# Performance work log

Hardware: AMD Instinct MI355X
Metric: run time of the kernel (lower is better)

## Reference

```python
import jax, jax.numpy as jnp
import numpy as np

B, N, IN, E, H, F = 64, 256, 128, 256, 8, 1024


def setup_inputs() -> dict:
    key = jax.random.key(0)
    ks = jax.random.split(key, 16)
    x = jax.random.normal(ks[0], (B, N, IN), jnp.float32)
    adj = (jax.random.uniform(ks[1], (B, N, N)) < 0.1).astype(jnp.float32)
    adj = jnp.maximum(adj, adj.transpose(0, 2, 1))  # symmetric 0/1 adjacency
    mask = jax.random.randint(ks[2], (B, N), 0, 2).astype(jnp.float32)
    dist = jax.random.normal(ks[3], (B, N, N), jnp.float32)

    def lin(k, i, o):
        return (jax.random.normal(k, (i, o), jnp.float32) / np.sqrt(i)).astype(jnp.float32)

    return dict(
        x=x, adj=adj, mask=mask, dist=dist,
        W1=lin(ks[4], IN, E), b1=jnp.zeros((E,), jnp.float32),
        W2=lin(ks[5], E, E), b2=jnp.zeros((E,), jnp.float32),
        W3=lin(ks[6], E, E), b3=jnp.zeros((E,), jnp.float32),
        ln1_g=jnp.ones((E,), jnp.float32), ln1_b=jnp.zeros((E,), jnp.float32),
        Wq=lin(ks[7], E, H * E), Wk=lin(ks[8], E, H * E), Wv=lin(ks[9], E, H * E),
        Wo=lin(ks[10], H * E, E), bo=jnp.zeros((E,), jnp.float32),
        ln2_g=jnp.ones((E,), jnp.float32), ln2_b=jnp.zeros((E,), jnp.float32),
        Wf1=lin(ks[11], E, F), bf1=jnp.zeros((F,), jnp.float32),
        Wf2=lin(ks[12], F, E), bf2=jnp.zeros((E,), jnp.float32),
    )


def _layernorm(x, g, b):
    m = x.mean(-1, keepdims=True)
    v = ((x - m) ** 2).mean(-1, keepdims=True)
    return (x - m) * jax.lax.rsqrt(v + 1e-5) * g + b


def reference(x, adj, mask, dist, W1, b1, W2, b2, W3, b3, ln1_g, ln1_b,
              Wq, Wk, Wv, Wo, bo, ln2_g, ln2_b, Wf1, bf1, Wf2, bf2):
    # --- DenseGCNConv normalization (add self-loops, sym-normalize) ---
    eye = jnp.eye(N, dtype=adj.dtype)
    A = adj * (1.0 - eye) + eye                      # fill_diag(adj, 1)
    dis = jax.lax.rsqrt(jnp.clip(A.sum(-1), 1.0, None))
    An = dis[:, :, None] * A * dis[:, None, :]       # D^-1/2 A D^-1/2, [B,N,N]
    m3 = mask[:, :, None]

    def gcn(h, W, b):
        return (jnp.einsum('bij,bjf->bif', An, h @ W) + b) * m3

    g1 = jax.nn.relu(gcn(x, W1, b1))
    g2 = jax.nn.relu(gcn(g1, W2, b2))
    g3 = jax.nn.relu(gcn(g2, W3, b3))
    gcn_res = g1 + g2 + g3

    # --- masked MHA with distance bias (head dim = E per head) ---
    h = _layernorm(gcn_res, ln1_g, ln1_b)
    mh = mask[:, None, :, None]                      # [B,1,N,1]
    q = (h @ Wq).reshape(B, N, H, E).transpose(0, 2, 1, 3) * mh
    k = (h @ Wk).reshape(B, N, H, E).transpose(0, 2, 1, 3) * mh
    v = (h @ Wv).reshape(B, N, H, E).transpose(0, 2, 1, 3) * mh
    a = jnp.einsum('bhne,bhme->bhnm', q * (E ** -0.5), k) + dist[:, None]
    am = (mask[:, :, None] * mask[:, None, :])[:, None]  # [B,1,N,N]
    a = jnp.where(am == 0, -1e9, a)
    a = jax.nn.softmax(a, axis=-1)
    a = jnp.where(am == 0, 0.0, a)
    y = jnp.einsum('bhnm,bhme->bhne', a, v).transpose(0, 2, 1, 3).reshape(B, N, H * E)
    y = (y @ Wo + bo) * m3
    att = gcn_res + y

    # --- FFN block ---
    f = _layernorm(att, ln2_g, ln2_b)
    f = (jax.nn.gelu(f @ Wf1 + bf1, approximate=False) @ Wf2 + bf2) * m3
    att = att + f
    return gcn_res + att
```

## Files before the change

kernel.cpp:

```cpp
#include <hip/hip_runtime.h>
#include <hip/hip_bf16.h>
#include <cmath>

#define BB 64
#define NNODES 256
#define INF_ 128
#define EE 256
#define HH 8
#define FFN 1024
#define BNROWS 16384

typedef __attribute__((ext_vector_type(8))) short short8;
typedef __attribute__((ext_vector_type(4))) float floatx4;
typedef __attribute__((ext_vector_type(4))) unsigned short ushort4v;

__device__ __forceinline__ float b2f(unsigned short u) {
  union { unsigned u32; float f; } w; w.u32 = ((unsigned)u) << 16; return w.f;
}
__device__ __forceinline__ unsigned short f2b(float f) {
  union { float f; unsigned u32; } w; w.f = f;
  unsigned r = w.u32 + 0x7FFFu + ((w.u32 >> 16) & 1u);
  return (unsigned short)(r >> 16);
}
__device__ __forceinline__ float gelu_f(float x) {
  const float z = 0.7978845608028654f * (x + 0.044715f * x * x * x);
  const float e = __expf(2.0f * z);
  const float th = (e - 1.0f) / (e + 1.0f);
  return 0.5f * x * (1.0f + th);
}

typedef const __attribute__((address_space(1))) void GV;
typedef __attribute__((address_space(3))) void LV;

__device__ __forceinline__ void gl_lds16(const unsigned short* g,
                                         unsigned short* l, int lane) {
#if __has_builtin(__builtin_amdgcn_global_load_lds)
  __builtin_amdgcn_global_load_lds((GV*)g, (LV*)l, 16, 0, 0);
#else
  *(short8*)(l + lane * 8) = *(const short8*)g;
#endif
}

struct PackArgs {
  const float* src[12];
  unsigned short* dst[12];
  int R[12], C[12];
  int start[13];
};

__launch_bounds__(256)
__global__ void pack_kernel(PackArgs a)
{
  __shared__ float tile[32][33];
  const int bid = blockIdx.x;
  int j = 0;
  while (bid >= a.start[j + 1]) j++;
  const int lb = bid - a.start[j];
  const float* src = a.src[j];
  unsigned short* dst = a.dst[j];
  const int R = a.R[j], C = a.C[j];

  if (C == 0) {
    const int i = (lb * 256 + threadIdx.x) * 4;
    if (i >= R) return;
    floatx4 v = *(const floatx4*)(src + i);
    ushort4v o;
    #pragma unroll
    for (int k = 0; k < 4; k++) o[k] = f2b(v[k]);
    *(ushort4v*)(dst + i) = o;
    return;
  }
  const int tpr = C >> 5;
  const int c0 = (lb % tpr) * 32, r0 = (lb / tpr) * 32;
  const int tx = threadIdx.x & 31, ty = threadIdx.x >> 5;
  #pragma unroll
  for (int i = ty; i < 32; i += 8)
    tile[i][tx] = src[(long long)(r0 + i) * C + c0 + tx];
  __syncthreads();
  #pragma unroll
  for (int i = ty; i < 32; i += 8)
    dst[(long long)(c0 + i) * R + r0 + tx] = f2b(tile[tx][i]);
}

__launch_bounds__(1024)
__global__ void an_kernel(const float* __restrict__ adj,
                          unsigned short* __restrict__ An)
{
  __shared__ float dis[256];
  const int b = blockIdx.x;
  const float* A = adj + (long long)b * 65536;
  const int t = threadIdx.x;
  const int row = t >> 2, seg = t & 3;
  const float* p = A + row * 256 + seg * 64;
  float s = 0.f;
  for (int k = 0; k < 64; k += 4) {
    floatx4 v = *(const floatx4*)(p + k);
    #pragma unroll
    for (int jj = 0; jj < 4; jj++) {
      const int col = seg * 64 + k + jj;
      s += (col == row) ? 1.0f : v[jj];
    }
  }
  s += __shfl_xor(s, 1);
  s += __shfl_xor(s, 2);
  if (seg == 0) dis[row] = 1.0f / sqrtf(fmaxf(s, 1.0f));
  __syncthreads();
  const float di = dis[row];
  unsigned short* dst = An + (long long)b * 65536 + row * 256 + seg * 64;
  for (int k = 0; k < 64; k += 4) {
    floatx4 v = *(const floatx4*)(p + k);
    ushort4v o;
    #pragma unroll
    for (int jj = 0; jj < 4; jj++) {
      const int col = seg * 64 + k + jj;
      o[jj] = f2b(di * dis[col] * ((col == row) ? 1.0f : v[jj]));
    }
    *(ushort4v*)(dst + k) = o;
  }
}

__launch_bounds__(512, 4)
__global__ void gemm_kernel(const unsigned short* __restrict__ A, int lda,
                            long long sAo, long long sAi,
                            const unsigned short* __restrict__ Bm, int ldb,
                            long long sBo, long long sBi,
                            void* __restrict__ Cv, int ldc,
                            long long sCo, long long sCi,
                            int K, int zshift, int mode, int flag,
                            const float* __restrict__ aux1,
                            const float* __restrict__ mask,
                            float* __restrict__ gcn,
                            void* __restrict__ aux2)
{
  __shared__ __align__(16) unsigned short sA[16384];
  __shared__ __align__(16) unsigned short sB[16384];

  const int t = threadIdx.x;
  const int z = blockIdx.z;
  const int zi = z & ((1 << zshift) - 1);
  const int zb = z >> zshift;
  const int m0 = blockIdx.x * 128;
  const int n0 = blockIdx.y * 128;
  A  += zb * sAo + zi * sAi;
  Bm += zb * sBo + zi * sBi;
  const long long cbase = zb * sCo + zi * sCi;

  const int lane = t & 63;
  const int w = t >> 6;
  const int wm = w >> 2, wn = w & 3;
  const int lm = lane & 15, qd = lane >> 4;

  floatx4 acc[4][2] = {};

  const int sub = lane >> 4;
  const int qs  = lane & 15;
  const unsigned short* pA[4];
  const unsigned short* pB[4];
  #pragma unroll
  for (int i = 0; i < 4; i++) {
    const int d = w * 4 + i;
    const int r = d * 4 + sub;
    const int co = (qs ^ (r & 7)) * 8;
    pA[i] = A + (long long)(m0 + r) * lda + co;
    pB[i] = Bm + (long long)(n0 + r) * ldb + co;
  }

  for (int kk = 0; kk < K; kk += 128) {
    #pragma unroll
    for (int i = 0; i < 4; i++) {
      gl_lds16(pA[i] + kk, &sA[(w * 4 + i) * 512], lane);
      gl_lds16(pB[i] + kk, &sB[(w * 4 + i) * 512], lane);
    }
    __syncthreads();

    #pragma unroll
    for (int ks = 0; ks < 4; ks++) {
      short8 af[4], bg[2];
      const int q = ks * 4 + qd;
      #pragma unroll
      for (int mi = 0; mi < 4; mi++) {
        const int r = wm * 64 + mi * 16 + lm;
        af[mi] = *(const short8*)&sA[r * 128 + ((q ^ (r & 7)) * 8)];
      }
      #pragma unroll
      for (int ni = 0; ni < 2; ni++) {
        const int r = wn * 32 + ni * 16 + lm;
        bg[ni] = *(const short8*)&sB[r * 128 + ((q ^ (r & 7)) * 8)];
      }
      #pragma unroll
      for (int mi = 0; mi < 4; mi++)
        #pragma unroll
        for (int ni = 0; ni < 2; ni++)
          acc[mi][ni] = __builtin_amdgcn_mfma_f32_16x16x32_bf16(
              af[mi], bg[ni], acc[mi][ni], 0, 0, 0);
    }
    __syncthreads();
  }

  #pragma unroll
  for (int mi = 0; mi < 4; mi++) {
    const int row0 = m0 + wm * 64 + mi * 16 + qd * 4;
    #pragma unroll
    for (int ni = 0; ni < 2; ni++) {
      const int col = n0 + wn * 32 + ni * 16 + lm;
      floatx4 a = acc[mi][ni];
      if (mode == 0) {
        float* Cf = (float*)Cv;
        #pragma unroll
        for (int r = 0; r < 4; r++)
          Cf[cbase + (long long)(row0 + r) * ldc + col] = a[r];
      } else if (mode == 1) {
        unsigned short* Cb = (unsigned short*)Cv;
        #pragma unroll
        for (int r = 0; r < 4; r++)
          Cb[cbase + (long long)(row0 + r) * ldc + col] = f2b(a[r]);
      } else if (mode == 2) {
        float* Cf = (float*)Cv;
        #pragma unroll
        for (int r = 0; r < 4; r++)
          Cf[cbase + (long long)(row0 + r) * ldc + col] += a[r];
      } else if (mode == 3) {
        unsigned short* Cb = (unsigned short*)Cv;
        const float bv = aux1[col];
        #pragma unroll
        for (int r = 0; r < 4; r++)
          Cb[cbase + (long long)(row0 + r) * ldc + col] = f2b(gelu_f(a[r] + bv));
      } else if (mode == 5) {
        const int b = row0 >> 8, n = row0 & 255;
        ushort4v o;
        #pragma unroll
        for (int r = 0; r < 4; r++) o[r] = f2b(a[r]);
        *(ushort4v*)((unsigned short*)Cv + (long long)b * 65536 + col * 256 + n) = o;
      } else if (mode == 8) {
        float* Cf = (float*)Cv;
        const float* attf = (const float*)aux2;
        const float bv = aux1[col];
        #pragma unroll
        for (int r = 0; r < 4; r++) {
          const long long idx = (long long)(row0 + r) * 256 + col;
          Cf[idx] = gcn[idx] + attf[idx] + (a[r] + bv) * mask[row0 + r];
        }
      } else if (mode == 9) {
        const int token = zb * 256 + col;
        const float m = mask[token];
        ushort4v o; floatx4 g;
        #pragma unroll
        for (int r = 0; r < 4; r++) {
          const float v = fmaxf((a[r] + aux1[row0 + r]) * m, 0.f);
          o[r] = f2b(v); g[r] = v;
        }
        *(ushort4v*)((unsigned short*)Cv + (long long)token * 256 + row0) = o;
        float* gp = gcn + (long long)token * 256 + row0;
        if (flag) { floatx4 old = *(const floatx4*)gp; g += old; }
        *(floatx4*)gp = g;
      } else if (mode == 12) {
        float* Cf = (float*)Cv;
        const float bv = aux1[col];
        #pragma unroll
        for (int r = 0; r < 4; r++) {
          const long long idx = (long long)(row0 + r) * 256 + col;
          Cf[idx] = gcn[idx] + (a[r] + bv) * mask[row0 + r];
        }
      } else if (mode == 13) {
        unsigned short* Cb = (unsigned short*)Cv;
        #pragma unroll
        for (int r = 0; r < 4; r++)
          Cb[cbase + (long long)(row0 + r) * ldc + col] = f2b(a[r] * 0.0625f);
      } else {
        if (col < 2048) {
          unsigned short* Cb = (unsigned short*)Cv;
          #pragma unroll
          for (int r = 0; r < 4; r++)
            Cb[(long long)(row0 + r) * 2048 + col] = f2b(a[r]);
        } else {
          const int z2 = (row0 >> 8) * 8 + ((col >> 8) - 8);
          const int e = col & 255, n = row0 & 255;
          ushort4v o;
          #pragma unroll
          for (int r = 0; r < 4; r++) o[r] = f2b(a[r]);
          *(ushort4v*)((unsigned short*)aux2 + (long long)z2 * 65536 + e * 256 + n) = o;
        }
      }
    }
  }
}

__launch_bounds__(512, 2)
__global__ void attn_kernel(unsigned short* __restrict__ QP,
                            const unsigned short* __restrict__ HBF,
                            const unsigned short* __restrict__ VT,
                            const unsigned short* __restrict__ DSTB,
                            const float* __restrict__ mask)
{
  __shared__ __align__(16) unsigned short sA8[8192];
  __shared__ __align__(16) unsigned short sB16[16384];
  __shared__ float redm[4][128];
  __shared__ float reds[4][128];

  const int mt = blockIdx.x;
  const int z  = blockIdx.y;
  const int b  = z >> 3, h = z & 7;
  const int t = threadIdx.x, lane = t & 63, w = t >> 6;
  const int wm = w >> 2, wn = w & 3;
  const int lm = lane & 15, qd = lane >> 4;
  const int m0 = mt * 128;

  unsigned short* Qm = QP + ((long long)(b * 256 + m0)) * 2048 + h * 256;
  const unsigned short* Hb = HBF + ((long long)b) * 65536;
  const unsigned short* Vb = VT + (long long)z * 65536;
  const unsigned short* db = DSTB + (long long)b * 65536;
  const float* maskb = mask + b * 256;

  const int rin = lane >> 3;
  const int qs  = lane & 7;

  floatx4 S[4][4] = {};
  for (int c = 0; c < 4; c++) {
    const int e0 = c * 64;
    #pragma unroll
    for (int i = 0; i < 2; i++) {
      const int d = w * 2 + i;
      const int r = d * 8 + rin;
      gl_lds16(Qm + (long long)r * 2048 + e0 + ((qs ^ (r & 7)) * 8),
               &sA8[d * 512], lane);
    }
    #pragma unroll
    for (int i = 0; i < 4; i++) {
      const int d = w * 4 + i;
      const int r = d * 8 + rin;
      gl_lds16(Hb + (long long)r * 256 + e0 + ((qs ^ (r & 7)) * 8),
               &sB16[d * 512], lane);
    }
    __syncthreads();
    #pragma unroll
    for (int ks = 0; ks < 2; ks++) {
      short8 af[4], bg4[4];
      const int o = ks * 4 + qd;
      #pragma unroll
      for (int mi = 0; mi < 4; mi++) {
        const int r = wm * 64 + mi * 16 + lm;
        af[mi] = *(const short8*)&sA8[r * 64 + ((o ^ (r & 7)) * 8)];
      }
      #pragma unroll
      for (int ni = 0; ni < 4; ni++) {
        const int r = wn * 64 + ni * 16 + lm;
        bg4[ni] = *(const short8*)&sB16[r * 64 + ((o ^ (r & 7)) * 8)];
      }
      #pragma unroll
      for (int mi = 0; mi < 4; mi++)
        #pragma unroll
        for (int ni = 0; ni < 4; ni++)
          S[mi][ni] = __builtin_amdgcn_mfma_f32_16x16x32_bf16(
              af[mi], bg4[ni], S[mi][ni], 0, 0, 0);
    }
    __syncthreads();
  }

  #pragma unroll
  for (int i = 0; i < 4; i++) {
    const int d = w * 4 + i;
    const int r = d * 8 + rin;
    gl_lds16(Vb + (long long)r * 256 + ((qs ^ (r & 7)) * 8),
             &sB16[d * 512], lane);
  }

  float mk[4];
  #pragma unroll
  for (int ni = 0; ni < 4; ni++) mk[ni] = maskb[wn * 64 + ni * 16 + lm];

  float lred[4][4];
  #pragma unroll
  for (int mi = 0; mi < 4; mi++) {
    #pragma unroll
    for (int r = 0; r < 4; r++) {
      const int row = wm * 64 + mi * 16 + qd * 4 + r;
      const float mq = maskb[m0 + row];
      float mx = -3e38f;
      #pragma unroll
      for (int ni = 0; ni < 4; ni++) {
        const int col = wn * 64 + ni * 16 + lm;
        const float dv = b2f(db[(long long)(m0 + row) * 256 + col]);
        const float v = (mq != 0.f && mk[ni] != 0.f) ? (S[mi][ni][r] + dv) : -1e9f;
        S[mi][ni][r] = v;
        mx = fmaxf(mx, v);
      }
      lred[mi][r] = mx;
    }
  }
  #pragma unroll
  for (int off = 1; off < 16; off <<= 1)
    #pragma unroll
    for (int mi = 0; mi < 4; mi++)
      #pragma unroll
      for (int r = 0; r < 4; r++)
        lred[mi][r] = fmaxf(lred[mi][r], __shfl_xor(lred[mi][r], off));
  if (lm == 0)
    #pragma unroll
    for (int mi = 0; mi < 4; mi++)
      #pragma unroll
      for (int r = 0; r < 4; r++)
        redm[wn][wm * 64 + mi * 16 + qd * 4 + r] = lred[mi][r];
  __syncthreads();

  #pragma unroll
  for (int mi = 0; mi < 4; mi++) {
    #pragma unroll
    for (int r = 0; r < 4; r++) {
      const int row = wm * 64 + mi * 16 + qd * 4 + r;
      const float gmax = fmaxf(fmaxf(redm[0][row], redm[1][row]),
                               fmaxf(redm[2][row], redm[3][row]));
      float s = 0.f;
      #pragma unroll
      for (int ni = 0; ni < 4; ni++) {
        const float e = __expf(S[mi][ni][r] - gmax);
        S[mi][ni][r] = e;
        s += e;
      }
      lred[mi][r] = s;
    }
  }
  #pragma unroll
  for (int off = 1; off < 16; off <<= 1)
    #pragma unroll
    for (int mi = 0; mi < 4; mi++)
      #pragma unroll
      for (int r = 0; r < 4; r++)
        lred[mi][r] += __shfl_xor(lred[mi][r], off);
  if (lm == 0)
    #pragma unroll
    for (int mi = 0; mi < 4; mi++)
      #pragma unroll
      for (int r = 0; r < 4; r++)
        reds[wn][wm * 64 + mi * 16 + qd * 4 + r] = lred[mi][r];
  __syncthreads();

  #pragma unroll
  for (int mi = 0; mi < 4; mi++) {
    #pragma unroll
    for (int r = 0; r < 4; r++) {
      const int row = wm * 64 + mi * 16 + qd * 4 + r;
      const float gs = reds[0][row] + reds[1][row] + reds[2][row] + reds[3][row];
      const float inv = 1.0f / gs;
      #pragma unroll
      for (int ni = 0; ni < 4; ni++) S[mi][ni][r] *= inv;
    }
  }

  floatx4 Y[4][4] = {};
  for (int c = 0; c < 4; c++) {
    if (wn == c) {
      #pragma unroll
      for (int mi = 0; mi < 4; mi++)
        #pragma unroll
        for (int r = 0; r < 4; r++) {
          const int row = wm * 64 + mi * 16 + qd * 4 + r;
          #pragma unroll
          for (int ni = 0; ni < 4; ni++) {
            const int kl = ni * 16 + lm;
            const int slot = (kl >> 3) ^ (row & 7);
            sA8[row * 64 + slot * 8 + (kl & 7)] = f2b(S[mi][ni][r]);
          }
        }
    }
    __syncthreads();
    #pragma unroll
    for (int ks = 0; ks < 2; ks++) {
      short8 af[4], bg4[4];
      const int o = ks * 4 + qd;
      #pragma unroll
      for (int mi = 0; mi < 4; mi++) {
        const int r = wm * 64 + mi * 16 + lm;
        af[mi] = *(const short8*)&sA8[r * 64 + ((o ^ (r & 7)) * 8)];
      }
      #pragma unroll
      for (int ni = 0; ni < 4; ni++) {
        const int r = wn * 64 + ni * 16 + lm;
        bg4[ni] = *(const short8*)&sB16[r * 64 + ((o ^ (r & 7)) * 8)];
      }
      #pragma unroll
      for (int mi = 0; mi < 4; mi++)
        #pragma unroll
        for (int ni = 0; ni < 4; ni++)
          Y[mi][ni] = __builtin_amdgcn_mfma_f32_16x16x32_bf16(
              af[mi], bg4[ni], Y[mi][ni], 0, 0, 0);
    }
    __syncthreads();
    if (c < 3) {
      #pragma unroll
      for (int i = 0; i < 4; i++) {
        const int d = w * 4 + i;
        const int r = d * 8 + rin;
        gl_lds16(Vb + (long long)r * 256 + (c + 1) * 64 + ((qs ^ (r & 7)) * 8),
                 &sB16[d * 512], lane);
      }
    }
  }

  #pragma unroll
  for (int mi = 0; mi < 4; mi++)
    #pragma unroll
    for (int ni = 0; ni < 4; ni++) {
      const int col = wn * 64 + ni * 16 + lm;
      #pragma unroll
      for (int r = 0; r < 4; r++) {
        const int row = wm * 64 + mi * 16 + qd * 4 + r;
        Qm[(long long)row * 2048 + col] = f2b(Y[mi][ni][r]);
      }
    }
}

__global__ void ln_kernel(const float* __restrict__ X,
                          const float* __restrict__ gam,
                          const float* __restrict__ bet,
                          unsigned short* __restrict__ out)
{
  const int g = blockIdx.x * 4 + (threadIdx.x >> 6);
  const int lane = threadIdx.x & 63;
  floatx4 v = *(const floatx4*)(X + (long long)g * 256 + lane * 4);
  float s = v[0] + v[1] + v[2] + v[3];
  float sq = v[0]*v[0] + v[1]*v[1] + v[2]*v[2] + v[3]*v[3];
  #pragma unroll
  for (int off = 32; off > 0; off >>= 1) {
    s  += __shfl_xor(s, off);
    sq += __shfl_xor(sq, off);
  }
  const float mean = s * (1.0f / 256.0f);
  const float var = sq * (1.0f / 256.0f) - mean * mean;
  const float rs = 1.0f / sqrtf(var + 1e-5f);
  ushort4v o;
  #pragma unroll
  for (int jj = 0; jj < 4; jj++) {
    const int c = lane * 4 + jj;
    o[jj] = f2b((v[jj] - mean) * rs * gam[c] + bet[c]);
  }
  *(ushort4v*)(out + (long long)g * 256 + lane * 4) = o;
}

static inline void launch_gemm(hipStream_t st, int M, int N, int batch,
    const void* A, int lda, long long sAo, long long sAi,
    const void* B, int ldb, long long sBo, long long sBi,
    void* C, int ldc, long long sCo, long long sCi,
    int K, int zshift, int mode, int flag,
    const float* aux1, const float* mask, float* gcn, void* aux2)
{
  dim3 grid(M / 128, N / 128, batch), blk(512);
  gemm_kernel<<<grid, blk, 0, st>>>(
      (const unsigned short*)A, lda, sAo, sAi,
      (const unsigned short*)B, ldb, sBo, sBi,
      C, ldc, sCo, sCi, K, zshift, mode, flag, aux1, mask, gcn, aux2);
}

extern "C" void kernel_launch(void* const* d_in, const int* in_sizes, int n_in,
                              void* d_out, int out_size, void* d_ws, size_t ws_size,
                              hipStream_t stream)
{
  (void)in_sizes; (void)n_in; (void)out_size;
  const float* x    = (const float*)d_in[0];
  const float* adj  = (const float*)d_in[1];
  const float* mask = (const float*)d_in[2];
  const float* dist = (const float*)d_in[3];
  const float* W1   = (const float*)d_in[4];
  const float* b1   = (const float*)d_in[5];
  const float* W2   = (const float*)d_in[6];
  const float* b2   = (const float*)d_in[7];
  const float* W3   = (const float*)d_in[8];
  const float* b3   = (const float*)d_in[9];
  const float* ln1g = (const float*)d_in[10];
  const float* ln1b = (const float*)d_in[11];
  const float* Wq   = (const float*)d_in[12];
  const float* Wk   = (const float*)d_in[13];
  const float* Wv   = (const float*)d_in[14];
  const float* Wo   = (const float*)d_in[15];
  const float* bo   = (const float*)d_in[16];
  const float* ln2g = (const float*)d_in[17];
  const float* ln2b = (const float*)d_in[18];
  const float* Wf1  = (const float*)d_in[19];
  const float* bf1  = (const float*)d_in[20];
  const float* Wf2  = (const float*)d_in[21];
  const float* bf2  = (const float*)d_in[22];

  char* w = (char*)d_ws;
  auto alloc = [&](size_t sz) { void* p = (void*)w; w += sz; return p; };
  unsigned short* W1T   = (unsigned short*)alloc(65536);
  unsigned short* W2T   = (unsigned short*)alloc(131072);
  unsigned short* W3T   = (unsigned short*)alloc(131072);
  unsigned short* ABH   = (unsigned short*)alloc(1048576);
  unsigned short* WVT   = (unsigned short*)alloc(1048576);
  unsigned short* WOT   = (unsigned short*)alloc(1048576);
  unsigned short* WF1T  = (unsigned short*)alloc(524288);
  unsigned short* WF2T  = (unsigned short*)alloc(524288);
  unsigned short* WQb   = (unsigned short*)alloc(1048576);
  unsigned short* WKb   = (unsigned short*)alloc(1048576);
  unsigned short* XBF   = (unsigned short*)alloc(4194304);
  unsigned short* DSTB  = (unsigned short*)alloc(8388608);
  float*          GCN   = (float*)         alloc(16777216);
  float*          U     = (float*)         alloc(16777216);
  unsigned short* HBF   = (unsigned short*)alloc(8388608);
  char* scratch = (char*)alloc(134217728);
  if ((size_t)(w - (char*)d_ws) > ws_size) return;
  unsigned short* AN  = (unsigned short*)scratch;
  unsigned short* TT  = (unsigned short*)(scratch + 8388608);
  unsigned short* GBF = (unsigned short*)(scratch + 16777216);
  unsigned short* QPB = (unsigned short*)scratch;
  unsigned short* VT  = (unsigned short*)(scratch + 67108864);
  unsigned short* FFB = (unsigned short*)scratch;

  PackArgs pa;
  const float* srcs[11] = {W1, W2, W3, Wv, Wo, Wf1, Wf2, x, Wq, Wk, dist};
  unsigned short* dsts[11] = {W1T, W2T, W3T, WVT, WOT, WF1T, WF2T, XBF, WQb, WKb, DSTB};
  const int Rs[11] = {128, 256, 256, 256, 2048, 256, 1024,
                      BNROWS * INF_, EE * HH * EE, EE * HH * EE, BB * 65536};
  const int Cs[11] = {256, 256, 256, 2048, 256, 1024, 256, 0, 0, 0, 0};
  const int sts[12] = {0, 32, 96, 160, 672, 1184, 1440, 1696, 3744, 4256, 4768, 8864};
  for (int j = 0; j < 11; j++) {
    pa.src[j] = srcs[j]; pa.dst[j] = dsts[j]; pa.R[j] = Rs[j]; pa.C[j] = Cs[j];
  }
  for (int j = 0; j < 12; j++) pa.start[j] = sts[j];
  pack_kernel<<<8864, 256, 0, stream>>>(pa);

  an_kernel<<<64, 1024, 0, stream>>>(adj, AN);

  launch_gemm(stream, 256, 256, 8, WKb, 2048, 256, 0, WQb, 2048, 256, 0,
              ABH, 256, 65536, 0, 256, 0, 13, 0, nullptr, nullptr, nullptr, nullptr);

  launch_gemm(stream, BNROWS, EE, 1, XBF, 128, 0,0, W1T, 128, 0,0,
              TT, 256, 0,0, 128, 0, 5, 0, nullptr, nullptr, nullptr, nullptr);
  launch_gemm(stream, 256, 256, BB, TT, 256, 65536,0, AN, 256, 65536,0,
              GBF, 256, 0,0, 256, 0, 9, 0, b1, mask, GCN, nullptr);
  launch_gemm(stream, BNROWS, EE, 1, GBF, 256, 0,0, W2T, 256, 0,0,
              TT, 256, 0,0, 256, 0, 5, 0, nullptr, nullptr, nullptr, nullptr);
  launch_gemm(stream, 256, 256, BB, TT, 256, 65536,0, AN, 256, 65536,0,
              GBF, 256, 0,0, 256, 0, 9, 1, b2, mask, GCN, nullptr);
  launch_gemm(stream, BNROWS, EE, 1, GBF, 256, 0,0, W3T, 256, 0,0,
              TT, 256, 0,0, 256, 0, 5, 0, nullptr, nullptr, nullptr, nullptr);
  launch_gemm(stream, 256, 256, BB, TT, 256, 65536,0, AN, 256, 65536,0,
              GBF, 256, 0,0, 256, 0, 9, 1, b3, mask, GCN, nullptr);

  ln_kernel<<<4096, 256, 0, stream>>>(GCN, ln1g, ln1b, HBF);

  launch_gemm(stream, BNROWS, 4096, 1, HBF, 256, 0,0, ABH, 256, 0,0,
              QPB, 2048, 0,0, 256, 0, 15, 0, nullptr, nullptr, nullptr, VT);
  attn_kernel<<<dim3(2, 512), 512, 0, stream>>>(QPB, HBF, VT, DSTB, mask);
  launch_gemm(stream, BNROWS, EE, 1, QPB, 2048, 0,0, WOT, 2048, 0,0,
              U, 256, 0,0, 2048, 0, 12, 0, bo, mask, GCN, nullptr);

  ln_kernel<<<4096, 256, 0, stream>>>(U, ln2g, ln2b, HBF);
  launch_gemm(stream, BNROWS, FFN, 1, HBF, 256, 0,0, WF1T, 256, 0,0,
              FFB, 1024, 0,0, 256, 0, 3, 0, bf1, nullptr, nullptr, nullptr);
  launch_gemm(stream, BNROWS, EE, 1, FFB, 1024, 0,0, WF2T, 1024, 0,0,
              d_out, 256, 0,0, 1024, 0, 8, 0, bf2, mask, GCN, U);
}
```

Before: 520.0 us.

## Split adjacency normalization into two wide kernels and shrink attention row tile

The single 64-block adjacency normalization kernel becomes a degree kernel followed by an elementwise normalize kernel, each launched with 4096 blocks to fill the GPU. The attention kernel now processes 64 query rows per block instead of 128, doubling the grid and cutting per-thread accumulators. Its output is staged through LDS so the stores to global memory are coalesced 16-byte writes. The trade-offs are an extra launch and a reread of the adjacency matrix, plus K/V tiles being loaded twice as often per head.

```diff
diff --git a/kernel.cpp b/kernel.cpp
--- a/kernel.cpp
+++ b/kernel.cpp
@@ -82,41 +82,43 @@
     dst[(long long)(c0 + i) * R + r0 + tx] = f2b(tile[tx][i]);
 }
 
-__launch_bounds__(1024)
+__global__ void deg_kernel(const float* __restrict__ adj,
+                           float* __restrict__ dis)
+{
+  const int g = blockIdx.x * 4 + (threadIdx.x >> 6);
+  const int lane = threadIdx.x & 63;
+  const int i = g & 255;
+  floatx4 v = *(const floatx4*)(adj + (long long)g * 256 + lane * 4);
+  float s = 0.f;
+  #pragma unroll
+  for (int jj = 0; jj < 4; jj++) {
+    const int j = lane * 4 + jj;
+    s += (j == i) ? 1.0f : v[jj];
+  }
+  #pragma unroll
+  for (int off = 32; off > 0; off >>= 1) s += __shfl_xor(s, off);
+  if (lane == 0) dis[g] = 1.0f / sqrtf(fmaxf(s, 1.0f));
+}
+
 __global__ void an_kernel(const float* __restrict__ adj,
+                          const float* __restrict__ dis,
                           unsigned short* __restrict__ An)
 {
-  __shared__ float dis[256];
-  const int b = blockIdx.x;
-  const float* A = adj + (long long)b * 65536;
-  const int t = threadIdx.x;
-  const int row = t >> 2, seg = t & 3;
-  const float* p = A + row * 256 + seg * 64;
-  float s = 0.f;
-  for (int k = 0; k < 64; k += 4) {
-    floatx4 v = *(const floatx4*)(p + k);
-    #pragma unroll
-    for (int jj = 0; jj < 4; jj++) {
-      const int col = seg * 64 + k + jj;
-      s += (col == row) ? 1.0f : v[jj];
-    }
-  }
-  s += __shfl_xor(s, 1);
-  s += __shfl_xor(s, 2);
-  if (seg == 0) dis[row] = 1.0f / sqrtf(fmaxf(s, 1.0f));
-  __syncthreads();
-  const float di = dis[row];
-  unsigned short* dst = An + (long long)b * 65536 + row * 256 + seg * 64;
-  for (int k = 0; k < 64; k += 4) {
-    floatx4 v = *(const floatx4*)(p + k);
-    ushort4v o;
-    #pragma unroll
-    for (int jj = 0; jj < 4; jj++) {
-      const int col = seg * 64 + k + jj;
-      o[jj] = f2b(di * dis[col] * ((col == row) ? 1.0f : v[jj]));
-    }
-    *(ushort4v*)(dst + k) = o;
-  }
+  const long long base = ((long long)blockIdx.x * 256 + threadIdx.x) * 4;
+  const int rowg = (int)(base >> 8);
+  const int i = rowg & 255;
+  const int brow = rowg & ~255;
+  const int j0 = (int)(base & 255);
+  const float di = dis[rowg];
+  floatx4 v = *(const floatx4*)(adj + base);
+  ushort4v o;
+  #pragma unroll
+  for (int jj = 0; jj < 4; jj++) {
+    const int j = j0 + jj;
+    const float a = (j == i) ? 1.0f : v[jj];
+    o[jj] = f2b(di * dis[brow + j] * a);
+  }
+  *(ushort4v*)(An + base) = o;
 }
 
 __launch_bounds__(512, 4)
@@ -292,10 +294,10 @@
                             const unsigned short* __restrict__ DSTB,
                             const float* __restrict__ mask)
 {
-  __shared__ __align__(16) unsigned short sA8[8192];
-  __shared__ __align__(16) unsigned short sB16[16384];
-  __shared__ float redm[4][128];
-  __shared__ float reds[4][128];
+  __shared__ __align__(16) unsigned short sQ[4096];
+  __shared__ __align__(16) unsigned short sKV[16896];
+  __shared__ float redm[4][64];
+  __shared__ float reds[4][64];
 
   const int mt = blockIdx.x;
   const int z  = blockIdx.y;
@@ -303,10 +305,10 @@
   const int t = threadIdx.x, lane = t & 63, w = t >> 6;
   const int wm = w >> 2, wn = w & 3;
   const int lm = lane & 15, qd = lane >> 4;
-  const int m0 = mt * 128;
+  const int m0 = mt * 64;
 
   unsigned short* Qm = QP + ((long long)(b * 256 + m0)) * 2048 + h * 256;
-  const unsigned short* Hb = HBF + ((long long)b) * 65536;
+  const unsigned short* Hb = HBF + (long long)b * 65536;
   const unsigned short* Vb = VT + (long long)z * 65536;
   const unsigned short* db = DSTB + (long long)b * 65536;
   const float* maskb = mask + b * 256;
@@ -314,40 +316,38 @@
   const int rin = lane >> 3;
   const int qs  = lane & 7;
 
-  floatx4 S[4][4] = {};
+  floatx4 S[2][4] = {};
   for (int c = 0; c < 4; c++) {
     const int e0 = c * 64;
-    #pragma unroll
-    for (int i = 0; i < 2; i++) {
-      const int d = w * 2 + i;
-      const int r = d * 8 + rin;
+    {
+      const int r = w * 8 + rin;
       gl_lds16(Qm + (long long)r * 2048 + e0 + ((qs ^ (r & 7)) * 8),
-               &sA8[d * 512], lane);
+               &sQ[w * 512], lane);
     }
     #pragma unroll
     for (int i = 0; i < 4; i++) {
       const int d = w * 4 + i;
       const int r = d * 8 + rin;
       gl_lds16(Hb + (long long)r * 256 + e0 + ((qs ^ (r & 7)) * 8),
-               &sB16[d * 512], lane);
+               &sKV[d * 512], lane);
     }
     __syncthreads();
     #pragma unroll
     for (int ks = 0; ks < 2; ks++) {
-      short8 af[4], bg4[4];
+      short8 af[2], bg4[4];
       const int o = ks * 4 + qd;
       #pragma unroll
-      for (int mi = 0; mi < 4; mi++) {
-        const int r = wm * 64 + mi * 16 + lm;
-        af[mi] = *(const short8*)&sA8[r * 64 + ((o ^ (r & 7)) * 8)];
+      for (int mi = 0; mi < 2; mi++) {
+        const int r = wm * 32 + mi * 16 + lm;
+        af[mi] = *(const short8*)&sQ[r * 64 + ((o ^ (r & 7)) * 8)];
       }
       #pragma unroll
       for (int ni = 0; ni < 4; ni++) {
         const int r = wn * 64 + ni * 16 + lm;
-        bg4[ni] = *(const short8*)&sB16[r * 64 + ((o ^ (r & 7)) * 8)];
-      }
-      #pragma unroll
-      for (int mi = 0; mi < 4; mi++)
+        bg4[ni] = *(const short8*)&sKV[r * 64 + ((o ^ (r & 7)) * 8)];
+      }
+      #pragma unroll
+      for (int mi = 0; mi < 2; mi++)
         #pragma unroll
         for (int ni = 0; ni < 4; ni++)
           S[mi][ni] = __builtin_amdgcn_mfma_f32_16x16x32_bf16(
@@ -361,19 +361,19 @@
     const int d = w * 4 + i;
     const int r = d * 8 + rin;
     gl_lds16(Vb + (long long)r * 256 + ((qs ^ (r & 7)) * 8),
-             &sB16[d * 512], lane);
+             &sKV[d * 512], lane);
   }
 
   float mk[4];
   #pragma unroll
   for (int ni = 0; ni < 4; ni++) mk[ni] = maskb[wn * 64 + ni * 16 + lm];
 
-  float lred[4][4];
-  #pragma unroll
-  for (int mi = 0; mi < 4; mi++) {
+  float lred[2][4];
+  #pragma unroll
+  for (int mi = 0; mi < 2; mi++) {
     #pragma unroll
     for (int r = 0; r < 4; r++) {
-      const int row = wm * 64 + mi * 16 + qd * 4 + r;
+      const int row = wm * 32 + mi * 16 + qd * 4 + r;
       const float mq = maskb[m0 + row];
       float mx = -3e38f;
       #pragma unroll
@@ -390,23 +390,23 @@
   #pragma unroll
   for (int off = 1; off < 16; off <<= 1)
     #pragma unroll
-    for (int mi = 0; mi < 4; mi++)
+    for (int mi = 0; mi < 2; mi++)
       #pragma unroll
       for (int r = 0; r < 4; r++)
         lred[mi][r] = fmaxf(lred[mi][r], __shfl_xor(lred[mi][r], off));
   if (lm == 0)
     #pragma unroll
-    for (int mi = 0; mi < 4; mi++)
+    for (int mi = 0; mi < 2; mi++)
       #pragma unroll
       for (int r = 0; r < 4; r++)
-        redm[wn][wm * 64 + mi * 16 + qd * 4 + r] = lred[mi][r];
+        redm[wn][wm * 32 + mi * 16 + qd * 4 + r] = lred[mi][r];
   __syncthreads();
 
   #pragma unroll
-  for (int mi = 0; mi < 4; mi++) {
+  for (int mi = 0; mi < 2; mi++) {
     #pragma unroll
     for (int r = 0; r < 4; r++) {
-      const int row = wm * 64 + mi * 16 + qd * 4 + r;
+      const int row = wm * 32 + mi * 16 + qd * 4 + r;
       const float gmax = fmaxf(fmaxf(redm[0][row], redm[1][row]),
                                fmaxf(redm[2][row], redm[3][row]));
       float s = 0.f;
@@ -422,23 +422,23 @@
   #pragma unroll
   for (int off = 1; off < 16; off <<= 1)
     #pragma unroll
-    for (int mi = 0; mi < 4; mi++)
+    for (int mi = 0; mi < 2; mi++)
       #pragma unroll
       for (int r = 0; r < 4; r++)
         lred[mi][r] += __shfl_xor(lred[mi][r], off);
   if (lm == 0)
     #pragma unroll
-    for (int mi = 0; mi < 4; mi++)
+    for (int mi = 0; mi < 2; mi++)
       #pragma unroll
       for (int r = 0; r < 4; r++)
-        reds[wn][wm * 64 + mi * 16 + qd * 4 + r] = lred[mi][r];
+        reds[wn][wm * 32 + mi * 16 + qd * 4 + r] = lred[mi][r];
   __syncthreads();
 
   #pragma unroll
-  for (int mi = 0; mi < 4; mi++) {
+  for (int mi = 0; mi < 2; mi++) {
     #pragma unroll
     for (int r = 0; r < 4; r++) {
-      const int row = wm * 64 + mi * 16 + qd * 4 + r;
+      const int row = wm * 32 + mi * 16 + qd * 4 + r;
       const float gs = reds[0][row] + reds[1][row] + reds[2][row] + reds[3][row];
       const float inv = 1.0f / gs;
       #pragma unroll
@@ -446,39 +446,39 @@
     }
   }
 
-  floatx4 Y[4][4] = {};
+  floatx4 Y[2][4] = {};
   for (int c = 0; c < 4; c++) {
     if (wn == c) {
       #pragma unroll
-      for (int mi = 0; mi < 4; mi++)
+      for (int mi = 0; mi < 2; mi++)
         #pragma unroll
         for (int r = 0; r < 4; r++) {
-          const int row = wm * 64 + mi * 16 + qd * 4 + r;
+          const int row = wm * 32 + mi * 16 + qd * 4 + r;
           #pragma unroll
           for (int ni = 0; ni < 4; ni++) {
             const int kl = ni * 16 + lm;
             const int slot = (kl >> 3) ^ (row & 7);
-            sA8[row * 64 + slot * 8 + (kl & 7)] = f2b(S[mi][ni][r]);
+            sQ[row * 64 + slot * 8 + (kl & 7)] = f2b(S[mi][ni][r]);
           }
         }
     }
     __syncthreads();
     #pragma unroll
     for (int ks = 0; ks < 2; ks++) {
-      short8 af[4], bg4[4];
+      short8 af[2], bg4[4];
       const int o = ks * 4 + qd;
       #pragma unroll
-      for (int mi = 0; mi < 4; mi++) {
-        const int r = wm * 64 + mi * 16 + lm;
-        af[mi] = *(const short8*)&sA8[r * 64 + ((o ^ (r & 7)) * 8)];
+      for (int mi = 0; mi < 2; mi++) {
+        const int r = wm * 32 + mi * 16 + lm;
+        af[mi] = *(const short8*)&sQ[r * 64 + ((o ^ (r & 7)) * 8)];
       }
       #pragma unroll
       for (int ni = 0; ni < 4; ni++) {
         const int r = wn * 64 + ni * 16 + lm;
-        bg4[ni] = *(const short8*)&sB16[r * 64 + ((o ^ (r & 7)) * 8)];
-      }
-      #pragma unroll
-      for (int mi = 0; mi < 4; mi++)
+        bg4[ni] = *(const short8*)&sKV[r * 64 + ((o ^ (r & 7)) * 8)];
+      }
+      #pragma unroll
+      for (int mi = 0; mi < 2; mi++)
         #pragma unroll
         for (int ni = 0; ni < 4; ni++)
           Y[mi][ni] = __builtin_amdgcn_mfma_f32_16x16x32_bf16(
@@ -491,22 +491,30 @@
         const int d = w * 4 + i;
         const int r = d * 8 + rin;
         gl_lds16(Vb + (long long)r * 256 + (c + 1) * 64 + ((qs ^ (r & 7)) * 8),
-                 &sB16[d * 512], lane);
-      }
-    }
-  }
-
-  #pragma unroll
-  for (int mi = 0; mi < 4; mi++)
+                 &sKV[d * 512], lane);
+      }
+    }
+  }
+
+  #pragma unroll
+  for (int mi = 0; mi < 2; mi++)
     #pragma unroll
     for (int ni = 0; ni < 4; ni++) {
       const int col = wn * 64 + ni * 16 + lm;
       #pragma unroll
       for (int r = 0; r < 4; r++) {
-        const int row = wm * 64 + mi * 16 + qd * 4 + r;
-        Qm[(long long)row * 2048 + col] = f2b(Y[mi][ni][r]);
-      }
-    }
+        const int row = wm * 32 + mi * 16 + qd * 4 + r;
+        sKV[row * 264 + col] = f2b(Y[mi][ni][r]);
+      }
+    }
+  __syncthreads();
+  #pragma unroll
+  for (int it = 0; it < 4; it++) {
+    const int idx = it * 512 + t;
+    const int row = idx >> 5, u = idx & 31;
+    short8 v = *(const short8*)&sKV[row * 264 + u * 8];
+    *(short8*)(Qm + (long long)row * 2048 + u * 8) = v;
+  }
 }
 
 __global__ void ln_kernel(const float* __restrict__ X,
@@ -596,6 +604,7 @@
   float*          GCN   = (float*)         alloc(16777216);
   float*          U     = (float*)         alloc(16777216);
   unsigned short* HBF   = (unsigned short*)alloc(8388608);
+  float*          DIS   = (float*)         alloc(65536);
   char* scratch = (char*)alloc(134217728);
   if ((size_t)(w - (char*)d_ws) > ws_size) return;
   unsigned short* AN  = (unsigned short*)scratch;
@@ -618,7 +627,8 @@
   for (int j = 0; j < 12; j++) pa.start[j] = sts[j];
   pack_kernel<<<8864, 256, 0, stream>>>(pa);
 
-  an_kernel<<<64, 1024, 0, stream>>>(adj, AN);
+  deg_kernel<<<4096, 256, 0, stream>>>(adj, DIS);
+  an_kernel<<<4096, 256, 0, stream>>>(adj, DIS, AN);
 
   launch_gemm(stream, 256, 256, 8, WKb, 2048, 256, 0, WQb, 2048, 256, 0,
               ABH, 256, 65536, 0, 256, 0, 13, 0, nullptr, nullptr, nullptr, nullptr);
@@ -640,7 +650,7 @@
 
   launch_gemm(stream, BNROWS, 4096, 1, HBF, 256, 0,0, ABH, 256, 0,0,
               QPB, 2048, 0,0, 256, 0, 15, 0, nullptr, nullptr, nullptr, VT);
-  attn_kernel<<<dim3(2, 512), 512, 0, stream>>>(QPB, HBF, VT, DSTB, mask);
+  attn_kernel<<<dim3(4, 512), 512, 0, stream>>>(QPB, HBF, VT, DSTB, mask);
   launch_gemm(stream, BNROWS, EE, 1, QPB, 2048, 0,0, WOT, 2048, 0,0,
               U, 256, 0,0, 2048, 0, 12, 0, bo, mask, GCN, nullptr);
 
```

After: 524.9 us. No clear change (+0.9%).
